# Kernel optimization log

Hardware: AMD Instinct MI355X
Metric: run time of the kernel (lower is better)

Reference implementation:

```python
import jax, jax.numpy as jnp
from jax import lax
import numpy as np

SEQ, BATCH, X_DIM = 256, 64, 64
FEAT = 256      # dense_x[-1]
DEC = 256       # dense_h_x[-1]
H = 512         # dim_rnn


def setup_inputs() -> dict:
    key = jax.random.key(0)
    ks = jax.random.split(key, 12)
    s = 0.05
    return {
        "x": jax.random.normal(ks[0], (SEQ, BATCH, X_DIM), jnp.float32),
        "mode_selector": jax.random.uniform(ks[1], (SEQ,), jnp.float32),
        # feature extractor: Linear(x_dim -> FEAT) + tanh
        "W_fx": jax.random.normal(ks[2], (FEAT, X_DIM), jnp.float32) * s,
        "b_fx": jnp.zeros((FEAT,), jnp.float32),
        # LSTM (single layer): gates ordered i, f, g, o (torch convention)
        "W_ih": jax.random.normal(ks[3], (4 * H, FEAT), jnp.float32) * s,
        "W_hh": jax.random.normal(ks[4], (4 * H, H), jnp.float32) * s,
        "b_ih": jnp.zeros((4 * H,), jnp.float32),
        "b_hh": jnp.zeros((4 * H,), jnp.float32),
        # decoder MLP: Linear(H -> DEC) + tanh
        "W_hx": jax.random.normal(ks[5], (DEC, H), jnp.float32) * s,
        "b_hx": jnp.zeros((DEC,), jnp.float32),
        # gen_out: Linear(DEC -> x_dim)
        "W_out": jax.random.normal(ks[6], (X_DIM, DEC), jnp.float32) * s,
        "b_out": jnp.zeros((X_DIM,), jnp.float32),
    }


def _forward(x, mode_selector, W_fx, b_fx, W_ih, W_hh, b_ih, b_hh,
             W_hx, b_hx, W_out, b_out):
    def fe(v):  # feature_extractor_x (dropout_p=0 -> identity)
        return jnp.tanh(v @ W_fx.T + b_fx)

    def gen(h):  # mlp_h_x + gen_out
        return jnp.tanh(h @ W_hx.T + b_hx) @ W_out.T + b_out

    def lstm_cell(feat, h, c):
        g = feat @ W_ih.T + b_ih + h @ W_hh.T + b_hh  # [B, 4H]
        i, f, gg, o = jnp.split(g, 4, axis=-1)
        c2 = jax.nn.sigmoid(f) * c + jax.nn.sigmoid(i) * jnp.tanh(gg)
        h2 = jax.nn.sigmoid(o) * jnp.tanh(c2)
        return h2, c2

    S, B, _ = x.shape
    feat_x = fe(x)  # [S, B, FEAT] teacher-forced features
    h0 = jnp.zeros((B, H), x.dtype)
    c0 = jnp.zeros((B, H), x.dtype)
    y0 = jnp.zeros((B, W_out.shape[0]), x.dtype)

    def step(carry, inp):
        h, c, y_prev = carry
        feat_tf, mix, is_first = inp
        # at t=0 original uses feature_x[0] as the "auto" feature
        feat_auto = jnp.where(is_first, feat_tf, fe(y_prev))
        feat = mix * feat_auto + (1.0 - mix) * feat_tf
        y_t = gen(h)           # generated from pre-update hidden state
        h2, c2 = lstm_cell(feat, h, c)
        return (h2, c2, y_t), y_t

    is_first = (jnp.arange(S) == 0)
    _, y = lax.scan(step, (h0, c0, y0), (feat_x, mode_selector, is_first))
    return y  # [S, B, x_dim]


def reference(x, mode_selector, W_fx, b_fx, W_ih, W_hh, b_ih, b_hh,
              W_hx, b_hx, W_out, b_out):
    return _forward(x, mode_selector, W_fx, b_fx, W_ih, W_hh, b_ih, b_hh,
                    W_hx, b_hx, W_out, b_out)
```

## Files before the change

### kernel.cpp

```cpp
#include <hip/hip_runtime.h>
#include <stdint.h>

typedef unsigned short u16;
typedef unsigned int u32;
typedef unsigned long long u64;
typedef __attribute__((ext_vector_type(8))) short short8;
typedef __attribute__((ext_vector_type(4))) float f32x4;
typedef __attribute__((ext_vector_type(4))) int int4v;

#define SEQ 256
#define GATE_WGS 64
#define D_WGS 4
#define NWG 69
#define A_ELE 49152
#define D_ELE 16384

__device__ __forceinline__ u16 f2bf(float f) {
  u32 u = __float_as_uint(f);
  u += 0x7FFFu + ((u >> 16) & 1u);
  return (u16)(u >> 16);
}
__device__ __forceinline__ float bf2f(u16 v) {
  return __uint_as_float(((u32)v) << 16);
}
__device__ __forceinline__ short8 cvt8(const float* __restrict__ p) {
  short8 r;
#pragma unroll
  for (int j = 0; j < 8; ++j) r[j] = (short)f2bf(p[j]);
  return r;
}
__device__ __forceinline__ short8 cvt8v(const float* __restrict__ p) {
  f32x4 a = *(const f32x4*)p, b = *(const f32x4*)(p + 4);
  short8 r;
#pragma unroll
  for (int j = 0; j < 4; ++j) { r[j] = (short)f2bf(a[j]); r[4 + j] = (short)f2bf(b[j]); }
  return r;
}
__device__ __forceinline__ float fast_tanh(float x) {
  return 1.0f - 2.0f / (1.0f + __expf(2.0f * x));
}
__device__ __forceinline__ float fast_sig(float x) {
  return 1.0f / (1.0f + __expf(-x));
}

union V16 { short8 s; u64 q[2]; };
__device__ __forceinline__ short8 ldc16(const u16* p) {
  V16 v;
  v.q[0] = __hip_atomic_load((const u64*)p,     __ATOMIC_RELAXED, __HIP_MEMORY_SCOPE_AGENT);
  v.q[1] = __hip_atomic_load((const u64*)p + 1, __ATOMIC_RELAXED, __HIP_MEMORY_SCOPE_AGENT);
  return v.s;
}
__device__ __forceinline__ void stc16(u16* p, const u64* s) {
  __hip_atomic_store((u64*)p,     s[0], __ATOMIC_RELAXED, __HIP_MEMORY_SCOPE_AGENT);
  __hip_atomic_store((u64*)p + 1, s[1], __ATOMIC_RELAXED, __HIP_MEMORY_SCOPE_AGENT);
}
__device__ __forceinline__ void pollge(u32* p, u32 v) {
  while (__hip_atomic_load(p, __ATOMIC_RELAXED, __HIP_MEMORY_SCOPE_AGENT) < v) {}
}
#define VMCNT0() asm volatile("s_waitcnt vmcnt(0)" ::: "memory")

__global__ void prep_misc(const float* __restrict__ W_fx, const float* __restrict__ b_fx,
                          const float* __restrict__ W_out, const float* __restrict__ b_out,
                          const float* __restrict__ W_hx,
                          u16* __restrict__ Abuf0, u32* __restrict__ flags,
                          float* __restrict__ bcomb, u16* __restrict__ Wcpack,
                          u16* __restrict__ Whx_pack) {
  int b = blockIdx.x, tid = threadIdx.x;
  if (b == 0) {
    for (int it = 0; it < 16; ++it) {
      int chunk = it * 256 + tid;
      *(int4v*)(Abuf0 + (2048 + chunk) * 8) = (int4v){0, 0, 0, 0};
    }
  } else if (b == 1) {
    for (int k = 0; k < 6; ++k) flags[k * 256 + tid] = 0u;
  } else if (b == 2) {
    float s = b_fx[tid];
    for (int k = 0; k < 64; ++k) s += W_fx[tid * 64 + k] * b_out[k];
    bcomb[tid] = s;
  } else if (b < 19) {
    int ct = b - 3;
    for (int it = 0; it < 16; ++it) {
      int o = it * 256 + tid;
      int cl = o >> 8, dec = o & 255;
      int c = ct * 16 + cl;
      float s = 0.f;
      for (int k = 0; k < 64; ++k) s += W_fx[c * 64 + k] * W_out[k * 256 + dec];
      int dwk = dec >> 5, kd = dec & 31;
      int l = (c & 15) + ((kd >> 3) << 4), j = kd & 7;
      Wcpack[((dwk * 16 + (c >> 4)) * 64 + l) * 8 + j] = f2bf(s);
    }
  } else {
    int base = (b - 19) * 2048;
#pragma unroll
    for (int it = 0; it < 8; ++it) {
      int cid = base + it * 256 + tid;
      int kb = cid >> 10, rem = cid & 1023, nt16 = rem >> 6, l = rem & 63;
      int row = nt16 * 16 + (l & 15);
      int k = kb * 32 + ((l >> 4) << 3);
      *(short8*)(Whx_pack + cid * 8) = cvt8v(W_hx + row * 512 + k);
    }
  }
}

__global__ void prep_ftf(const float* __restrict__ x, const float* __restrict__ W_fx,
                         const float* __restrict__ b_fx, u16* __restrict__ ftf) {
  __shared__ __attribute__((aligned(16))) u16 fstage[64 * 264];
  const int t = blockIdx.x, tid = threadIdx.x;
  const int wv = tid >> 6, ln = tid & 63;
  const int c15 = ln & 15, qq = ln >> 4;
  short8 WfR[2][4];
#pragma unroll
  for (int kk = 0; kk < 2; ++kk)
#pragma unroll
    for (int nt = 0; nt < 4; ++nt)
      WfR[kk][nt] = cvt8(W_fx + ((wv * 4 + nt) * 16 + c15) * 64 + kk * 32 + qq * 8);
  float bfx_r[4];
#pragma unroll
  for (int nt = 0; nt < 4; ++nt) bfx_r[nt] = b_fx[(wv * 4 + nt) * 16 + c15];
  short8 xa[2][4];
#pragma unroll
  for (int kb = 0; kb < 2; ++kb)
#pragma unroll
    for (int mt = 0; mt < 4; ++mt)
      xa[kb][mt] = cvt8v(x + (t * 64 + mt * 16 + c15) * 64 + kb * 32 + qq * 8);
  f32x4 tf[4][4];
#pragma unroll
  for (int nt = 0; nt < 4; ++nt)
#pragma unroll
    for (int mt = 0; mt < 4; ++mt) tf[nt][mt] = (f32x4){0.f, 0.f, 0.f, 0.f};
#pragma unroll
  for (int kb = 0; kb < 2; ++kb)
#pragma unroll
    for (int nt = 0; nt < 4; ++nt)
#pragma unroll
      for (int mt = 0; mt < 4; ++mt)
        tf[nt][mt] = __builtin_amdgcn_mfma_f32_16x16x32_bf16(xa[kb][mt], WfR[kb][nt], tf[nt][mt], 0, 0, 0);
#pragma unroll
  for (int nt = 0; nt < 4; ++nt)
#pragma unroll
    for (int mt = 0; mt < 4; ++mt)
#pragma unroll
      for (int r2 = 0; r2 < 4; ++r2) {
        int row = mt * 16 + qq * 4 + r2;
        fstage[row * 264 + (wv * 4 + nt) * 16 + c15] = f2bf(fast_tanh(tf[nt][mt][r2] + bfx_r[nt]));
      }
  __syncthreads();
  u16* ftfb = ftf + t * 16384;
#pragma unroll
  for (int it = 0; it < 8; ++it) {
    int chunk = it * 256 + tid;
    int kb = chunk >> 8, l = chunk & 63;
    int m = ((chunk >> 6) & 3) * 16 + (l & 15);
    int k = kb * 32 + (l >> 4) * 8;
    *(short8*)(ftfb + chunk * 8) = *(const short8*)(fstage + m * 264 + k);
  }
}

__global__ void __launch_bounds__(256, 1)
rnn_kernel(const float* __restrict__ x, const float* __restrict__ msel,
           const float* __restrict__ W_ih, const float* __restrict__ W_hh,
           const float* __restrict__ b_ih, const float* __restrict__ b_hh,
           const float* __restrict__ b_hx,
           const float* __restrict__ W_out, const float* __restrict__ b_out,
           float* __restrict__ out,
           u16* __restrict__ Abase, u16* __restrict__ dbase,
           u32* __restrict__ flags,
           const float* __restrict__ bcomb, const u16* __restrict__ Wcpack,
           const u16* __restrict__ Whx_pack,
           const u16* __restrict__ ftf, u16* __restrict__ fblend) {
  __shared__ __attribute__((aligned(16))) char smem[109568];
  const int wgid = blockIdx.x;
  const int tid = threadIdx.x;
  const int wv = tid >> 6, ln = tid & 63;
  u32* hcnt  = flags + 1168;
  u32* dcnt  = flags + 1232;
  u32* fbcnt = flags + 1296;

  if (wgid < GATE_WGS) {
    const int wg = wgid;
    float* red = (float*)smem;
    u16* hstage = (u16*)(smem + 32768);
    short8 Breg[6][2];
#pragma unroll
    for (int kk = 0; kk < 6; ++kk) {
      int kb = wv + kk * 4;
#pragma unroll
      for (int nt = 0; nt < 2; ++nt) {
        int n = ln & 15, q = ln >> 4;
        int gate = nt * 2 + (n >> 3), unit = n & 7;
        int row = gate * 512 + wg * 8 + unit;
        int k = kb * 32 + q * 8;
        const float* src = (k < 256) ? (W_ih + row * 256 + k) : (W_hh + row * 512 + (k - 256));
        Breg[kk][nt] = cvt8(src);
      }
    }
    float bsum_r[2][4];
#pragma unroll
    for (int it = 0; it < 2; ++it) {
      int u = (it * 256 + tid) & 7;
#pragma unroll
      for (int g = 0; g < 4; ++g) {
        int row = g * 512 + wg * 8 + u;
        bsum_r[it][g] = b_ih[row] + b_hh[row];
      }
    }
    float creg[2] = {0.f, 0.f};
    const int kbW = 8 + (wg >> 2), qW = wg & 3;
    int r = 0, rn = 1;
    for (int t = 0; t < SEQ; ++t) {
      if (tid < 4) pollge(&hcnt[tid * 16], (u32)(16 * t));
      __syncthreads();
      const u16* A = Abase + r * A_ELE;
      u16* An = Abase + rn * A_ELE;
      f32x4 acc[2][4];
#pragma unroll
      for (int nt = 0; nt < 2; nt++)
#pragma unroll
        for (int mt = 0; mt < 4; mt++) acc[nt][mt] = (f32x4){0.f, 0.f, 0.f, 0.f};
      short8 ah[4][4];
#pragma unroll
      for (int kk = 2; kk < 6; ++kk) {
        int kb = wv + kk * 4;
#pragma unroll
        for (int mt = 0; mt < 4; ++mt)
          ah[kk - 2][mt] = ldc16(A + ((kb * 4 + mt) * 64 + ln) * 8);
      }
#pragma unroll
      for (int kk = 2; kk < 6; ++kk)
#pragma unroll
        for (int nt = 0; nt < 2; nt++)
#pragma unroll
          for (int mt = 0; mt < 4; mt++)
            acc[nt][mt] = __builtin_amdgcn_mfma_f32_16x16x32_bf16(ah[kk - 2][mt], Breg[kk][nt], acc[nt][mt], 0, 0, 0);
      if (tid == 64 && t > 0) pollge(&fbcnt[(t & 1) * 16], 4u * ((u32)(t + 1) >> 1));
      __syncthreads();
      {
        const u16* fsrc = (t == 0) ? ftf : (fblend + (t & 1) * 16384);
#pragma unroll
        for (int kk = 0; kk < 2; ++kk) {
          int kb = wv + kk * 4;
          short8 af[4];
#pragma unroll
          for (int mt = 0; mt < 4; ++mt)
            af[mt] = ldc16(fsrc + ((kb * 4 + mt) * 64 + ln) * 8);
#pragma unroll
          for (int nt = 0; nt < 2; nt++)
#pragma unroll
            for (int mt = 0; mt < 4; mt++)
              acc[nt][mt] = __builtin_amdgcn_mfma_f32_16x16x32_bf16(af[mt], Breg[kk][nt], acc[nt][mt], 0, 0, 0);
        }
      }
#pragma unroll
      for (int nt = 0; nt < 2; nt++)
#pragma unroll
        for (int mt = 0; mt < 4; mt++)
          *(f32x4*)(red + ((wv * 8 + nt * 4 + mt) * 64 + ln) * 4) = acc[nt][mt];
      __syncthreads();
#pragma unroll
      for (int it = 0; it < 2; ++it) {
        int item = it * 256 + tid;
        int m = item >> 3, u = item & 7;
        int mt = m >> 4, lq = ((m & 15) >> 2) * 16, reg = m & 3;
        float g4[4];
#pragma unroll
        for (int g = 0; g < 4; ++g) {
          float s = bsum_r[it][g];
          int base = ((g >> 1) * 4 + mt) * 64 + lq + (g & 1) * 8 + u;
#pragma unroll
          for (int w = 0; w < 4; ++w) s += red[(w * 8 * 64 + base) * 4 + reg];
          g4[g] = s;
        }
        float ii = fast_sig(g4[0]), ff = fast_sig(g4[1]);
        float gg = fast_tanh(g4[2]), oo = fast_sig(g4[3]);
        float cn = ff * creg[it] + ii * gg;
        creg[it] = cn;
        float h = oo * fast_tanh(cn);
        hstage[(mt * 16 + (m & 15)) * 8 + u] = f2bf(h);
      }
      __syncthreads();
      if (tid < 64) {
        int mt2 = tid >> 4, m15 = tid & 15;
        u16* dst = An + (((kbW * 4 + mt2) * 64 + qW * 16 + m15) * 8);
        stc16(dst, (const u64*)(hstage + tid * 8));
        VMCNT0();
        if (tid == 0)
          (void)__hip_atomic_fetch_add(&hcnt[(wg & 3) * 16], 1u,
                                       __ATOMIC_RELAXED, __HIP_MEMORY_SCOPE_AGENT);
      }
      r = rn; rn = (rn == 2) ? 0 : rn + 1;
    }
  } else if (wgid < GATE_WGS + D_WGS) {
    const int dw = wgid - GATE_WGS;
    u16* dstage = (u16*)smem;
    float* fstg = (float*)(smem + 8448);
    float bhx_r[4];
#pragma unroll
    for (int ntl = 0; ntl < 4; ++ntl) bhx_r[ntl] = b_hx[(wv * 4 + ntl) * 16 + (ln & 15)];
    int r = 0, rn = 1;
    for (int t = 0; t < SEQ; ++t) {
      if (tid < 4) pollge(&hcnt[tid * 16], (u32)(16 * t));
      __syncthreads();
      const u16* A = Abase + r * A_ELE;
      u16* dbufR = dbase + (t & 3) * D_ELE;
      short8 ah[16];
#pragma unroll
      for (int kbh = 0; kbh < 16; ++kbh)
        ah[kbh] = ldc16(A + (((8 + kbh) * 4 + dw) * 64 + ln) * 8);
      f32x4 acc[4];
#pragma unroll
      for (int ntl = 0; ntl < 4; ++ntl) acc[ntl] = (f32x4){0.f, 0.f, 0.f, 0.f};
#pragma unroll
      for (int kbh = 0; kbh < 16; ++kbh) {
#pragma unroll
        for (int ntl = 0; ntl < 4; ++ntl) {
          short8 bw = *(const short8*)(Whx_pack + ((kbh * 16 + wv * 4 + ntl) * 64 + ln) * 8);
          acc[ntl] = __builtin_amdgcn_mfma_f32_16x16x32_bf16(ah[kbh], bw, acc[ntl], 0, 0, 0);
        }
      }
#pragma unroll
      for (int ntl = 0; ntl < 4; ++ntl)
#pragma unroll
        for (int reg = 0; reg < 4; ++reg)
          dstage[((ln >> 4) * 4 + reg) * 264 + (wv * 4 + ntl) * 16 + (ln & 15)]
              = f2bf(fast_tanh(acc[ntl][reg] + bhx_r[ntl]));
      __syncthreads();
#pragma unroll
      for (int s = 0; s < 2; ++s) {
        int cl = s * 256 + tid;
        int kd = cl >> 6, l = cl & 63;
        V16 v; v.s = *(const short8*)(dstage + (l & 15) * 264 + kd * 32 + (l >> 4) * 8);
        stc16(dbufR + ((kd * 4 + dw) * 64 + l) * 8, v.q);
      }
      if (t < SEQ - 1) {
        f32x4 acc2[4];
#pragma unroll
        for (int ntf = 0; ntf < 4; ++ntf) acc2[ntf] = (f32x4){0.f, 0.f, 0.f, 0.f};
#pragma unroll
        for (int kd = 0; kd < 8; ++kd) {
          short8 ad = *(const short8*)(dstage + (ln & 15) * 264 + kd * 32 + (ln >> 4) * 8);
#pragma unroll
          for (int ntf = 0; ntf < 4; ++ntf) {
            short8 bw = *(const short8*)(Wcpack + ((kd * 16 + wv * 4 + ntf) * 64 + ln) * 8);
            acc2[ntf] = __builtin_amdgcn_mfma_f32_16x16x32_bf16(ad, bw, acc2[ntf], 0, 0, 0);
          }
        }
#pragma unroll
        for (int ntf = 0; ntf < 4; ++ntf)
#pragma unroll
          for (int reg = 0; reg < 4; ++reg)
            fstg[((ln >> 4) * 4 + reg) * 264 + (wv * 4 + ntf) * 16 + (ln & 15)] = acc2[ntf][reg];
        __syncthreads();
        float mixg = msel[t + 1];
        const u16* ftfb = ftf + (t + 1) * 16384;
        u16* fbl = fblend + ((t + 1) & 1) * 16384;
#pragma unroll
        for (int s = 0; s < 2; ++s) {
          int cl = s * 256 + tid;
          int kb = cl >> 6, l = cl & 63;
          int c0 = kb * 32 + (l >> 4) * 8;
          const float* fr = fstg + (l & 15) * 264 + c0;
          short8 tfv = *(const short8*)(ftfb + ((kb * 4 + dw) * 64 + l) * 8);
          short8 rr;
#pragma unroll
          for (int j = 0; j < 8; ++j) {
            float av = fr[j] + bcomb[c0 + j];
            rr[j] = (short)f2bf(mixg * fast_tanh(av) + (1.f - mixg) * bf2f((u16)tfv[j]));
          }
          V16 v; v.s = rr;
          stc16(fbl + ((kb * 4 + dw) * 64 + l) * 8, v.q);
        }
        VMCNT0();
        __syncthreads();
        if (tid == 0) {
          (void)__hip_atomic_fetch_add(dcnt, 1u, __ATOMIC_RELAXED, __HIP_MEMORY_SCOPE_AGENT);
          (void)__hip_atomic_fetch_add(&fbcnt[((t + 1) & 1) * 16], 1u,
                                       __ATOMIC_RELAXED, __HIP_MEMORY_SCOPE_AGENT);
        }
      } else {
        VMCNT0();
        __syncthreads();
        if (tid == 0)
          (void)__hip_atomic_fetch_add(dcnt, 1u, __ATOMIC_RELAXED, __HIP_MEMORY_SCOPE_AGENT);
      }
      r = rn; rn = (rn == 2) ? 0 : rn + 1;
    }
  } else {
    float* red = (float*)smem;
    const int c15 = ln & 15, qq = ln >> 4;
    short8 WoR[2][4];
#pragma unroll
    for (int kk = 0; kk < 2; ++kk) {
      int koffo = (wv * 2 + kk) * 32 + qq * 8;
#pragma unroll
      for (int nt = 0; nt < 4; ++nt)
        WoR[kk][nt] = cvt8(W_out + (nt * 16 + c15) * 256 + koffo);
    }
    float bout_r = b_out[wv * 16 + c15];
    for (int t = 0; t < SEQ; ++t) {
      if (tid == 0) pollge(dcnt, 4u * (u32)(t + 1));
      __syncthreads();
      const u16* dbufR = dbase + (t & 3) * D_ELE;
      short8 da[2][4];
#pragma unroll
      for (int kk = 0; kk < 2; ++kk)
#pragma unroll
        for (int mt = 0; mt < 4; ++mt)
          da[kk][mt] = ldc16(dbufR + (((wv * 2 + kk) * 4 + mt) * 64 + ln) * 8);
      f32x4 acc[4][4];
#pragma unroll
      for (int nt = 0; nt < 4; nt++)
#pragma unroll
        for (int mt = 0; mt < 4; mt++) acc[nt][mt] = (f32x4){0.f, 0.f, 0.f, 0.f};
#pragma unroll
      for (int kk = 0; kk < 2; ++kk)
#pragma unroll
        for (int nt = 0; nt < 4; nt++)
#pragma unroll
          for (int mt = 0; mt < 4; mt++)
            acc[nt][mt] = __builtin_amdgcn_mfma_f32_16x16x32_bf16(da[kk][mt], WoR[kk][nt], acc[nt][mt], 0, 0, 0);
#pragma unroll
      for (int nt = 0; nt < 4; nt++)
#pragma unroll
        for (int mt = 0; mt < 4; mt++)
          *(f32x4*)(red + ((wv * 16 + nt * 4 + mt) * 64 + ln) * 4) = acc[nt][mt];
      __syncthreads();
#pragma unroll
      for (int mt = 0; mt < 4; ++mt) {
        f32x4 s = (f32x4){0.f, 0.f, 0.f, 0.f};
#pragma unroll
        for (int w2 = 0; w2 < 4; ++w2)
          s += *(const f32x4*)(red + ((w2 * 16 + wv * 4 + mt) * 64 + ln) * 4);
#pragma unroll
        for (int r2 = 0; r2 < 4; ++r2) {
          int row = mt * 16 + qq * 4 + r2;
          out[t * 4096 + row * 64 + wv * 16 + c15] = s[r2] + bout_r;
        }
      }
      __syncthreads();
    }
  }
}

extern "C" void kernel_launch(void* const* d_in, const int* in_sizes, int n_in,
                              void* d_out, int out_size, void* d_ws, size_t ws_size,
                              hipStream_t stream) {
  const float* x     = (const float*)d_in[0];
  const float* msel  = (const float*)d_in[1];
  const float* W_fx  = (const float*)d_in[2];
  const float* b_fx  = (const float*)d_in[3];
  const float* W_ih  = (const float*)d_in[4];
  const float* W_hh  = (const float*)d_in[5];
  const float* b_ih  = (const float*)d_in[6];
  const float* b_hh  = (const float*)d_in[7];
  const float* W_hx  = (const float*)d_in[8];
  const float* b_hx  = (const float*)d_in[9];
  const float* W_out = (const float*)d_in[10];
  const float* b_out = (const float*)d_in[11];

  uint8_t* ws = (uint8_t*)d_ws;
  u16*   Abase    = (u16*)ws;
  u16*   dbase    = (u16*)(ws + 294912);
  u32*   flags    = (u32*)(ws + 425984);
  float* bcomb    = (float*)(ws + 432128);
  u16*   Wcpack   = (u16*)(ws + 433152);
  u16*   fblend   = (u16*)(ws + 564224);
  u16*   Whx_pack = (u16*)(ws + 629760);
  u16*   ftf      = (u16*)(ws + 891904);

  prep_misc<<<27, 256, 0, stream>>>(W_fx, b_fx, W_out, b_out, W_hx,
                                    Abase, flags, bcomb, Wcpack, Whx_pack);
  prep_ftf<<<256, 256, 0, stream>>>(x, W_fx, b_fx, ftf);
  rnn_kernel<<<NWG, 256, 0, stream>>>(x, msel, W_ih, W_hh, b_ih, b_hh,
                                      b_hx, W_out, b_out,
                                      (float*)d_out, Abase, dbase, flags,
                                      bcomb, Wcpack, Whx_pack, ftf, fblend);
}
```

Measured before the change: 2.299 ms.

## Split gate work by batch tile per wave and drop block-level syncs

Each gate workgroup now assigns each wave one 16-row batch tile, and that wave holds all 24 K-blocks of its weight slice in registers. Previously the K dimension was split across waves, which required an LDS reduction and several __syncthreads per step. Gate activations are now combined within a wave using lane shuffles, and each wave publishes its own h slice and increments the counter, so the expected counts become 64 per step. This removes the LDS reduction and block barriers from the recurrent critical path. The cost is much higher register pressure (48 short8 weight registers per lane) and four times more atomic counter traffic.

```diff
diff --git a/kernel.cpp b/kernel.cpp
--- a/kernel.cpp
+++ b/kernel.cpp
@@ -58,6 +58,7 @@
   while (__hip_atomic_load(p, __ATOMIC_RELAXED, __HIP_MEMORY_SCOPE_AGENT) < v) {}
 }
 #define VMCNT0() asm volatile("s_waitcnt vmcnt(0)" ::: "memory")
+#define LGKM0() asm volatile("s_waitcnt lgkmcnt(0)" ::: "memory")
 
 __global__ void prep_misc(const float* __restrict__ W_fx, const float* __restrict__ b_fx,
                           const float* __restrict__ W_out, const float* __restrict__ b_out,
@@ -178,12 +179,10 @@
 
   if (wgid < GATE_WGS) {
     const int wg = wgid;
-    float* red = (float*)smem;
-    u16* hstage = (u16*)(smem + 32768);
-    short8 Breg[6][2];
-#pragma unroll
-    for (int kk = 0; kk < 6; ++kk) {
-      int kb = wv + kk * 4;
+    u16* hstage = (u16*)smem;
+    short8 Breg[24][2];
+#pragma unroll
+    for (int kb = 0; kb < 24; ++kb)
 #pragma unroll
       for (int nt = 0; nt < 2; ++nt) {
         int n = ln & 15, q = ln >> 4;
@@ -191,102 +190,78 @@
         int row = gate * 512 + wg * 8 + unit;
         int k = kb * 32 + q * 8;
         const float* src = (k < 256) ? (W_ih + row * 256 + k) : (W_hh + row * 512 + (k - 256));
-        Breg[kk][nt] = cvt8(src);
-      }
-    }
-    float bsum_r[2][4];
-#pragma unroll
-    for (int it = 0; it < 2; ++it) {
-      int u = (it * 256 + tid) & 7;
-#pragma unroll
-      for (int g = 0; g < 4; ++g) {
-        int row = g * 512 + wg * 8 + u;
-        bsum_r[it][g] = b_ih[row] + b_hh[row];
-      }
-    }
-    float creg[2] = {0.f, 0.f};
+        Breg[kb][nt] = cvt8(src);
+      }
+    float bsum[2];
+    {
+      int n = ln & 15;
+#pragma unroll
+      for (int nt = 0; nt < 2; ++nt) {
+        int gate = nt * 2 + (n >> 3), unit = n & 7;
+        int row = gate * 512 + wg * 8 + unit;
+        bsum[nt] = b_ih[row] + b_hh[row];
+      }
+    }
+    f32x4 creg = (f32x4){0.f, 0.f, 0.f, 0.f};
     const int kbW = 8 + (wg >> 2), qW = wg & 3;
+    const int hi = (ln >> 3) & 1;
     int r = 0, rn = 1;
     for (int t = 0; t < SEQ; ++t) {
-      if (tid < 4) pollge(&hcnt[tid * 16], (u32)(16 * t));
-      __syncthreads();
+      if (ln < 4) pollge(&hcnt[ln * 16], (u32)(64 * t));
       const u16* A = Abase + r * A_ELE;
       u16* An = Abase + rn * A_ELE;
-      f32x4 acc[2][4];
-#pragma unroll
-      for (int nt = 0; nt < 2; nt++)
-#pragma unroll
-        for (int mt = 0; mt < 4; mt++) acc[nt][mt] = (f32x4){0.f, 0.f, 0.f, 0.f};
-      short8 ah[4][4];
-#pragma unroll
-      for (int kk = 2; kk < 6; ++kk) {
-        int kb = wv + kk * 4;
-#pragma unroll
-        for (int mt = 0; mt < 4; ++mt)
-          ah[kk - 2][mt] = ldc16(A + ((kb * 4 + mt) * 64 + ln) * 8);
-      }
-#pragma unroll
-      for (int kk = 2; kk < 6; ++kk)
-#pragma unroll
-        for (int nt = 0; nt < 2; nt++)
-#pragma unroll
-          for (int mt = 0; mt < 4; mt++)
-            acc[nt][mt] = __builtin_amdgcn_mfma_f32_16x16x32_bf16(ah[kk - 2][mt], Breg[kk][nt], acc[nt][mt], 0, 0, 0);
-      if (tid == 64 && t > 0) pollge(&fbcnt[(t & 1) * 16], 4u * ((u32)(t + 1) >> 1));
-      __syncthreads();
+      f32x4 acc0 = (f32x4){0.f, 0.f, 0.f, 0.f};
+      f32x4 acc1 = (f32x4){0.f, 0.f, 0.f, 0.f};
+      short8 ah[16];
+#pragma unroll
+      for (int kh = 0; kh < 16; ++kh)
+        ah[kh] = ldc16(A + (((8 + kh) * 4 + wv) * 64 + ln) * 8);
+#pragma unroll
+      for (int kh = 0; kh < 16; ++kh) {
+        acc0 = __builtin_amdgcn_mfma_f32_16x16x32_bf16(ah[kh], Breg[8 + kh][0], acc0, 0, 0, 0);
+        acc1 = __builtin_amdgcn_mfma_f32_16x16x32_bf16(ah[kh], Breg[8 + kh][1], acc1, 0, 0, 0);
+      }
+      if (ln == 4 && t > 0) pollge(&fbcnt[(t & 1) * 16], 4u * ((u32)(t + 1) >> 1));
       {
         const u16* fsrc = (t == 0) ? ftf : (fblend + (t & 1) * 16384);
-#pragma unroll
-        for (int kk = 0; kk < 2; ++kk) {
-          int kb = wv + kk * 4;
-          short8 af[4];
-#pragma unroll
-          for (int mt = 0; mt < 4; ++mt)
-            af[mt] = ldc16(fsrc + ((kb * 4 + mt) * 64 + ln) * 8);
-#pragma unroll
-          for (int nt = 0; nt < 2; nt++)
-#pragma unroll
-            for (int mt = 0; mt < 4; mt++)
-              acc[nt][mt] = __builtin_amdgcn_mfma_f32_16x16x32_bf16(af[mt], Breg[kk][nt], acc[nt][mt], 0, 0, 0);
-        }
-      }
-#pragma unroll
-      for (int nt = 0; nt < 2; nt++)
-#pragma unroll
-        for (int mt = 0; mt < 4; mt++)
-          *(f32x4*)(red + ((wv * 8 + nt * 4 + mt) * 64 + ln) * 4) = acc[nt][mt];
-      __syncthreads();
-#pragma unroll
-      for (int it = 0; it < 2; ++it) {
-        int item = it * 256 + tid;
-        int m = item >> 3, u = item & 7;
-        int mt = m >> 4, lq = ((m & 15) >> 2) * 16, reg = m & 3;
-        float g4[4];
-#pragma unroll
-        for (int g = 0; g < 4; ++g) {
-          float s = bsum_r[it][g];
-          int base = ((g >> 1) * 4 + mt) * 64 + lq + (g & 1) * 8 + u;
-#pragma unroll
-          for (int w = 0; w < 4; ++w) s += red[(w * 8 * 64 + base) * 4 + reg];
-          g4[g] = s;
-        }
-        float ii = fast_sig(g4[0]), ff = fast_sig(g4[1]);
-        float gg = fast_tanh(g4[2]), oo = fast_sig(g4[3]);
-        float cn = ff * creg[it] + ii * gg;
-        creg[it] = cn;
-        float h = oo * fast_tanh(cn);
-        hstage[(mt * 16 + (m & 15)) * 8 + u] = f2bf(h);
-      }
-      __syncthreads();
-      if (tid < 64) {
-        int mt2 = tid >> 4, m15 = tid & 15;
-        u16* dst = An + (((kbW * 4 + mt2) * 64 + qW * 16 + m15) * 8);
-        stc16(dst, (const u64*)(hstage + tid * 8));
-        VMCNT0();
-        if (tid == 0)
-          (void)__hip_atomic_fetch_add(&hcnt[(wg & 3) * 16], 1u,
-                                       __ATOMIC_RELAXED, __HIP_MEMORY_SCOPE_AGENT);
-      }
+        short8 af[8];
+#pragma unroll
+        for (int kf = 0; kf < 8; ++kf)
+          af[kf] = ldc16(fsrc + ((kf * 4 + wv) * 64 + ln) * 8);
+#pragma unroll
+        for (int kf = 0; kf < 8; ++kf) {
+          acc0 = __builtin_amdgcn_mfma_f32_16x16x32_bf16(af[kf], Breg[kf][0], acc0, 0, 0, 0);
+          acc1 = __builtin_amdgcn_mfma_f32_16x16x32_bf16(af[kf], Breg[kf][1], acc1, 0, 0, 0);
+        }
+      }
+      f32x4 h4;
+#pragma unroll
+      for (int reg = 0; reg < 4; ++reg) {
+        float g0 = acc0[reg] + bsum[0];
+        float g1 = acc1[reg] + bsum[1];
+        float p0 = __shfl_xor(g0, 8, 64);
+        float p1 = __shfl_xor(g1, 8, 64);
+        float iv = hi ? p0 : g0;
+        float fv = hi ? g0 : p0;
+        float gv = hi ? p1 : g1;
+        float ov = hi ? g1 : p1;
+        float cn = fast_sig(fv) * creg[reg] + fast_sig(iv) * fast_tanh(gv);
+        creg[reg] = cn;
+        h4[reg] = fast_sig(ov) * fast_tanh(cn);
+      }
+      if ((ln & 15) < 8) {
+#pragma unroll
+        for (int reg = 0; reg < 4; ++reg)
+          hstage[wv * 128 + ((ln >> 4) * 4 + reg) * 8 + (ln & 7)] = f2bf(h4[reg]);
+      }
+      LGKM0();
+      if (ln < 16)
+        stc16(An + (((kbW * 4 + wv) * 64 + qW * 16 + ln) * 8),
+              (const u64*)(hstage + wv * 128 + ln * 8));
+      VMCNT0();
+      if (ln == 0)
+        (void)__hip_atomic_fetch_add(&hcnt[(wg & 3) * 16], 1u,
+                                     __ATOMIC_RELAXED, __HIP_MEMORY_SCOPE_AGENT);
       r = rn; rn = (rn == 2) ? 0 : rn + 1;
     }
   } else if (wgid < GATE_WGS + D_WGS) {
@@ -298,7 +273,7 @@
     for (int ntl = 0; ntl < 4; ++ntl) bhx_r[ntl] = b_hx[(wv * 4 + ntl) * 16 + (ln & 15)];
     int r = 0, rn = 1;
     for (int t = 0; t < SEQ; ++t) {
-      if (tid < 4) pollge(&hcnt[tid * 16], (u32)(16 * t));
+      if (tid < 4) pollge(&hcnt[tid * 16], (u32)(64 * t));
       __syncthreads();
       const u16* A = Abase + r * A_ELE;
       u16* dbufR = dbase + (t & 3) * D_ELE;
```

Measured after the change: 2.507 ms. 1.09x slower.
